# Kernel tuning notes

Hardware: AMD Instinct MI355X
Metric: run time of the kernel (lower is better)

Reference implementation:

```python
import jax, jax.numpy as jnp
import numpy as np

WS = 3   # window_size
ND = 3   # n_degree


def grid_sample_bilinear(x, grid):
    """torch.nn.functional.grid_sample, mode='bilinear', padding_mode='zeros', align_corners=True.
    x: [B,C,H,W]; grid: [B,Hg,Wg,2] with grid[...,0]=x(norm), grid[...,1]=y(norm). -> [B,C,Hg,Wg]"""
    B, C, H, W = x.shape
    gx = (grid[..., 0] + 1.0) * 0.5 * (W - 1)
    gy = (grid[..., 1] + 1.0) * 0.5 * (H - 1)
    x0 = jnp.floor(gx); y0 = jnp.floor(gy)
    x1 = x0 + 1.0;      y1 = y0 + 1.0
    wx1 = gx - x0; wx0 = 1.0 - wx1
    wy1 = gy - y0; wy0 = 1.0 - wy1
    xf = x.reshape(B, C, H * W)

    def gather(yi, xi):
        valid = ((yi >= 0) & (yi <= H - 1) & (xi >= 0) & (xi <= W - 1)).astype(x.dtype)
        yc = jnp.clip(yi, 0, H - 1).astype(jnp.int32)
        xc = jnp.clip(xi, 0, W - 1).astype(jnp.int32)
        idx = yc * W + xc                                   # [B,Hg,Wg]
        v = jax.vmap(lambda xb, ib: jnp.take(xb, ib, axis=1))(xf, idx.reshape(B, -1))
        v = v.reshape(B, C, idx.shape[1], idx.shape[2])      # [B,C,Hg,Wg]
        return v * valid[:, None]

    out = (gather(y0, x0) * (wy0 * wx0)[:, None]
         + gather(y0, x1) * (wy0 * wx1)[:, None]
         + gather(y1, x0) * (wy1 * wx0)[:, None]
         + gather(y1, x1) * (wy1 * wx1)[:, None])
    return out


def setup_inputs() -> dict:
    key = jax.random.key(0)
    ks = jax.random.split(key, 8)
    B, Q, C, H, W = 16, 500, 256, 64, 64
    Np = ND + 1
    query = jax.random.normal(ks[0], (B, Q, C), dtype=jnp.float32)
    # polynomial coefficients kept small so most sample points land inside [-1,1]
    polys = jax.random.uniform(ks[1], (B, Q, 2 * Np), dtype=jnp.float32, minval=0.0, maxval=0.25)
    memory = jax.random.normal(ks[2], (B, H * W, C), dtype=jnp.float32)
    memory_spatial_shapes = np.array([[H, W]], dtype=np.int64)  # static shapes
    Wk = jax.random.normal(ks[3], (C, Np * C, WS, WS), dtype=jnp.float32) * 0.02
    bk = jax.random.normal(ks[4], (C,), dtype=jnp.float32) * 0.02
    Wp = jax.random.normal(ks[5], (C, C), dtype=jnp.float32) * 0.02
    bp = jax.random.normal(ks[6], (C,), dtype=jnp.float32) * 0.02
    return {"query": query, "polys": polys, "memory": memory,
            "memory_spatial_shapes": memory_spatial_shapes,
            "Wk": Wk, "bk": bk, "Wp": Wp, "bp": bp}


def reference(query, polys, memory, memory_spatial_shapes, Wk, bk, Wp, bp):
    B, LEN_V, C = memory.shape
    H = int(memory_spatial_shapes[0][0]); W = int(memory_spatial_shapes[0][1])
    Q = polys.shape[1]
    Np = ND + 1

    # memory -> feature map [B,C,H,W]
    x = jnp.transpose(memory[:, :H * W, :], (0, 2, 1)).reshape(B, C, H, W)

    # polynomial sample points: alphas[s,k] = linspace(0,1)[s] ** (ND-k)
    a = jnp.linspace(0.0, 1.0, Np).astype(polys.dtype)
    A = jnp.stack([a ** i for i in range(ND, -1, -1)], axis=1)          # [Np, Np]
    pts = jnp.einsum('bqck,sk->bqcs', polys.reshape(B, Q, 2, Np), A)    # [B,Q,2,Np]
    pts = jnp.transpose(pts, (0, 1, 3, 2))[..., ::-1]                   # [B,Q,Np,2] (flip coords)
    points = 2.0 * pts - 1.0
    points = points[:, :, None]                                         # [B,Q,1,Np,2]

    # window offsets (note python floor-div: (-3)//2 = -2, matches torch source)
    delta_h = 2.0 * jnp.linspace((-WS) // 2, WS // 2, WS) / H
    delta_w = 2.0 * jnp.linspace((-WS) // 2, WS // 2, WS) / W
    mesh_x, mesh_y = jnp.meshgrid(delta_w, delta_h, indexing='xy')       # [WS,WS]
    mesh_x = mesh_x.reshape(-1, 1); mesh_y = mesh_y.reshape(-1, 1)       # [WS*WS,1]

    grid_x = points[..., 1] + mesh_x                                     # [B,Q,WS*WS,Np]
    grid_y = points[..., 0] + mesh_y
    grid = jnp.stack((grid_y, grid_x), axis=-1)                          # [B,Q,WS*WS,Np,2]
    grid = grid.reshape(B, Q * Np * WS, WS, 2)

    sampled = grid_sample_bilinear(x, grid)                              # [B,C,Q*Np*WS,WS]
    sampled = sampled.reshape(B, C, Q * Np, WS, WS)
    sampled = jnp.transpose(sampled, (0, 2, 1, 3, 4)).reshape(B * Q, Np * C, WS, WS)

    # convkk over full window -> 1x1 output: plain contraction
    crcts = jax.nn.relu(jnp.einsum('nikl,oikl->no', sampled, Wk) + bk)   # [B*Q, C]
    crcts = (crcts @ Wp.T + bp).reshape(B, Q, C)
    return crcts, points
```

## Files before the change

### kernel.cpp

```cpp
#include <hip/hip_runtime.h>

#define NB 16
#define NQ 500
#define NC 256
#define NHW 64
#define MR 8000
#define KD 9216

typedef float f32x4 __attribute__((ext_vector_type(4)));
typedef __bf16 bf16x8 __attribute__((ext_vector_type(8)));
typedef unsigned short ushortx8 __attribute__((ext_vector_type(8)));
typedef unsigned int uintx4 __attribute__((ext_vector_type(4)));
typedef int intx4 __attribute__((ext_vector_type(4)));

__device__ __forceinline__ unsigned short f2bf(float f) {
  unsigned int u = __builtin_bit_cast(unsigned int, f);
  u += 0x7fffu + ((u >> 16) & 1u);
  return (unsigned short)(u >> 16);
}
#define U2F(u) __builtin_bit_cast(float, (unsigned int)(u))

__global__ void k_prep(const float* __restrict__ mem, unsigned short* __restrict__ memb,
                       const float* __restrict__ Wk, const float* __restrict__ Wp,
                       unsigned short* __restrict__ W2s, unsigned short* __restrict__ WPs,
                       const float* __restrict__ polys, float* __restrict__ outp,
                       float* __restrict__ wsp, float* __restrict__ wts) {
  const int bid = blockIdx.x;
  if (bid < 8192) {
    size_t gid = (size_t)bid * 256 + threadIdx.x;
    const float* s = mem + gid * 8;
    f32x4 a = *(const f32x4*)s, b = *(const f32x4*)(s + 4);
    bf16x8 pk;
    pk[0] = (__bf16)a.x; pk[1] = (__bf16)a.y; pk[2] = (__bf16)a.z; pk[3] = (__bf16)a.w;
    pk[4] = (__bf16)b.x; pk[5] = (__bf16)b.y; pk[6] = (__bf16)b.z; pk[7] = (__bf16)b.w;
    *(bf16x8*)(memb + gid * 8) = pk;
  } else if (bid < 9344) {
    int tid = (bid - 8192) * 256 + threadIdx.x;
    int o = tid & 255;
    int th = tid >> 8;
    int r = th >> 5;
    int cbase = (th & 31) * 8;
    int np = r / 9;
    int kl = r - np * 9;
    int kk = kl / 3;
    int ll = kl - kk * 3;
    const float* src = Wk + (size_t)o * KD + (size_t)(np * 256 + cbase) * 9 + kk * 3 + ll;
    ushortx8 v;
#pragma unroll
    for (int j = 0; j < 8; ++j) v[j] = f2bf(src[(size_t)j * 9]);
    *(ushortx8*)(W2s + (size_t)th * 2048 + o * 8) = v;
  } else if (bid < 9376) {
    int tid = (bid - 9344) * 256 + threadIdx.x;
    int o = tid & 255;
    int th = tid >> 8;
    const float* src = Wp + (size_t)o * 256 + th * 8;
    ushortx8 v;
#pragma unroll
    for (int j = 0; j < 8; ++j) v[j] = f2bf(src[j]);
    *(ushortx8*)(WPs + (size_t)th * 2048 + o * 8) = v;
  } else if (bid < 10501) {
    if (!wts) return;
    int e = (bid - 9376) * 256 + threadIdx.x;
    int r = e / 8000;
    int n = e - r * 8000;
    int s = r & 3;
    int mm = r >> 2;
    int mdiv = (mm * 11) >> 5;
    int mmod = mm - 3 * mdiv;
    float dhx = (1.5f * (float)mdiv - 2.0f) * 0.03125f;
    float dwy = (1.5f * (float)mmod - 2.0f) * 0.03125f;
    f32x4 ca = *(const f32x4*)(polys + (size_t)n * 8);
    f32x4 cb = *(const f32x4*)(polys + (size_t)n * 8 + 4);
    float a1 = (s == 3) ? 1.0f : (float)s * 0.33333334f;
    float a2 = a1 * a1, a3 = a2 * a1;
    float v0 = ca.x * a3 + ca.y * a2 + ca.z * a1 + ca.w;
    float v1 = cb.x * a3 + cb.y * a2 + cb.z * a1 + cb.w;
    float p0 = 2.0f * v1 - 1.0f;
    float p1 = 2.0f * v0 - 1.0f;
    const float gx = (p0 + dhx + 1.0f) * 0.5f * 63.0f;
    const float gy = (p1 + dwy + 1.0f) * 0.5f * 63.0f;
    const float x0f = floorf(gx), y0f = floorf(gy);
    const float fx = gx - x0f, fy = gy - y0f;
    const int ix0 = (int)x0f, iy0 = (int)y0f;
    const int ix1 = ix0 + 1, iy1 = iy0 + 1;
    const float vx0 = (ix0 >= 0 && ix0 < NHW) ? 1.0f : 0.0f;
    const float vx1 = (ix1 >= 0 && ix1 < NHW) ? 1.0f : 0.0f;
    const float vy0 = (iy0 >= 0 && iy0 < NHW) ? 1.0f : 0.0f;
    const float vy1 = (iy1 >= 0 && iy1 < NHW) ? 1.0f : 0.0f;
    const float w00 = (1.0f - fy) * (1.0f - fx) * vy0 * vx0;
    const float w01 = (1.0f - fy) * fx * vy0 * vx1;
    const float w10 = fy * (1.0f - fx) * vy1 * vx0;
    const float w11 = fy * fx * vy1 * vx1;
    const int cx0 = min(max(ix0, 0), NHW - 1), cx1 = min(max(ix1, 0), NHW - 1);
    const int cy0 = min(max(iy0, 0), NHW - 1), cy1 = min(max(iy1, 0), NHW - 1);
    float* dst = wts + (size_t)e * 8;
    f32x4 wv; wv.x = w00; wv.y = w01; wv.z = w10; wv.w = w11;
    intx4 ov;
    ov.x = (cy0 * NHW + cx0) * NC; ov.y = (cy0 * NHW + cx1) * NC;
    ov.z = (cy1 * NHW + cx0) * NC; ov.w = (cy1 * NHW + cx1) * NC;
    *(f32x4*)dst = wv;
    *(intx4*)(dst + 4) = ov;
  } else {
    int n = (bid - 10501) * 256 + threadIdx.x;
    if (n >= MR) return;
    f32x4 ca = *(const f32x4*)(polys + (size_t)n * 8);
    f32x4 cb = *(const f32x4*)(polys + (size_t)n * 8 + 4);
    const float av[4] = {0.0f, 0.33333334f, 0.66666669f, 1.0f};
#pragma unroll
    for (int s = 0; s < 4; ++s) {
      float a1 = av[s], a2 = a1 * a1, a3 = a2 * a1;
      float v0 = ca.x * a3 + ca.y * a2 + ca.z * a1 + ca.w;
      float v1 = cb.x * a3 + cb.y * a2 + cb.z * a1 + cb.w;
      float pt0 = 2.0f * v1 - 1.0f;
      float pt1 = 2.0f * v0 - 1.0f;
      outp[(size_t)n * 8 + s * 2 + 0] = pt0;
      outp[(size_t)n * 8 + s * 2 + 1] = pt1;
      wsp[(size_t)n * 8 + s * 2 + 0] = pt0;
      wsp[(size_t)n * 8 + s * 2 + 1] = pt1;
    }
  }
}

template <bool USE_WTS>
__global__ __launch_bounds__(512, 4) void k_gemm1(
    const unsigned short* __restrict__ memb, const float* __restrict__ pts,
    const float* __restrict__ wts, const unsigned short* __restrict__ W2s,
    const float* __restrict__ bk, float* __restrict__ PART, int K) {
  __shared__ __align__(16) unsigned short Alds[2 * 2048 * 8];
  __shared__ __align__(16) float Wlds[2][512];

  const int bid = blockIdx.x;
  const int x = bid & 7;
  const int kk8 = (bid >> 3) % K;
  const int j = bid / (8 * K);
  const int t = x + 8 * j;
  if (t >= 125) return;
  const int tt = 16 * x - ((x > 5) ? (x - 5) : 0) + j;
  const int nsl = 36 / K;
  const int r0 = kk8 * nsl;

  const int tid = threadIdx.x;
  const int n0 = tt * 64;
  const int lane = tid & 63;
  const int wave = tid >> 6;
  const int lr = lane & 15;
  const int ksub = lane >> 4;
  const int o0 = wave * 32;

  const int gchunk = tid & 31;
  const int gm0 = tid >> 5;

  size_t boff[4];
  int nrow[4];
#pragma unroll
  for (int task = 0; task < 4; ++task) {
    nrow[task] = n0 + gm0 + 16 * task;
    boff[task] = (size_t)(nrow[task] / NQ) * (NHW * NHW * NC);
  }

  f32x4 acc[4][2] = {};

  if (USE_WTS) {
    if (tid < 128) {
      f32x4 v = *(const f32x4*)(wts + ((size_t)r0 * 8000 + n0) * 8 + tid * 4);
      *(f32x4*)(&Wlds[0][tid * 4]) = v;
    }
    __syncthreads();
  }

  for (int r = r0; r < r0 + nsl; ++r) {
    const int lbase = ((r - r0) & 1) * 2048;
    const int cur = (r - r0) & 1;
    const int nbuf = cur ^ 1;
    const int rn = (r + 1 < 35) ? (r + 1) : 35;
    float dhx = 0.0f, dwy = 0.0f;
    int s = 0;
    if (!USE_WTS) {
      s = r & 3;
      const int mm = r >> 2;
      const int mdiv = (mm * 11) >> 5;
      const int mmod = mm - 3 * mdiv;
      dhx = (1.5f * (float)mdiv - 2.0f) * 0.03125f;
      dwy = (1.5f * (float)mmod - 2.0f) * 0.03125f;
    } else {
      if (tid < 128) {
        f32x4 v = *(const f32x4*)(wts + ((size_t)rn * 8000 + n0) * 8 + tid * 4);
        *(f32x4*)(&Wlds[nbuf][tid * 4]) = v;
      }
    }
#pragma unroll 2
    for (int task = 0; task < 4; ++task) {
      const int m = gm0 + task * 16;
      const int n = nrow[task];
      float w00, w01, w10, w11;
      int o00, o01, o10, o11;
      if (USE_WTS) {
        const float* we = &Wlds[cur][(gm0 + 16 * task) * 8];
        f32x4 wv = *(const f32x4*)we;
        intx4 ov = *(const intx4*)(we + 4);
        w00 = wv.x; w01 = wv.y; w10 = wv.z; w11 = wv.w;
        o00 = ov.x; o01 = ov.y; o10 = ov.z; o11 = ov.w;
      } else {
        const float p0 = pts[(size_t)n * 8 + s * 2 + 0];
        const float p1 = pts[(size_t)n * 8 + s * 2 + 1];
        const float gx = (p0 + dhx + 1.0f) * 0.5f * 63.0f;
        const float gy = (p1 + dwy + 1.0f) * 0.5f * 63.0f;
        const float x0f = floorf(gx), y0f = floorf(gy);
        const float fx = gx - x0f, fy = gy - y0f;
        const int ix0 = (int)x0f, iy0 = (int)y0f;
        const int ix1 = ix0 + 1, iy1 = iy0 + 1;
        const float vx0 = (ix0 >= 0 && ix0 < NHW) ? 1.0f : 0.0f;
        const float vx1 = (ix1 >= 0 && ix1 < NHW) ? 1.0f : 0.0f;
        const float vy0 = (iy0 >= 0 && iy0 < NHW) ? 1.0f : 0.0f;
        const float vy1 = (iy1 >= 0 && iy1 < NHW) ? 1.0f : 0.0f;
        w00 = (1.0f - fy) * (1.0f - fx) * vy0 * vx0;
        w01 = (1.0f - fy) * fx * vy0 * vx1;
        w10 = fy * (1.0f - fx) * vy1 * vx0;
        w11 = fy * fx * vy1 * vx1;
        const int cx0 = min(max(ix0, 0), NHW - 1), cx1 = min(max(ix1, 0), NHW - 1);
        const int cy0 = min(max(iy0, 0), NHW - 1), cy1 = min(max(iy1, 0), NHW - 1);
        o00 = (cy0 * NHW + cx0) * NC; o01 = (cy0 * NHW + cx1) * NC;
        o10 = (cy1 * NHW + cx0) * NC; o11 = (cy1 * NHW + cx1) * NC;
      }
      const unsigned short* mb = memb + boff[task] + gchunk * 8;
      uintx4 u00 = *(const uintx4*)(mb + o00);
      uintx4 u01 = *(const uintx4*)(mb + o01);
      uintx4 u10 = *(const uintx4*)(mb + o10);
      uintx4 u11 = *(const uintx4*)(mb + o11);
      f32x4 a00, b00, a01, b01, a10, b10, a11, b11;
      a00.x = U2F(u00.x << 16); a00.y = U2F(u00.x & 0xFFFF0000u);
      a00.z = U2F(u00.y << 16); a00.w = U2F(u00.y & 0xFFFF0000u);
      b00.x = U2F(u00.z << 16); b00.y = U2F(u00.z & 0xFFFF0000u);
      b00.z = U2F(u00.w << 16); b00.w = U2F(u00.w & 0xFFFF0000u);
      a01.x = U2F(u01.x << 16); a01.y = U2F(u01.x & 0xFFFF0000u);
      a01.z = U2F(u01.y << 16); a01.w = U2F(u01.y & 0xFFFF0000u);
      b01.x = U2F(u01.z << 16); b01.y = U2F(u01.z & 0xFFFF0000u);
      b01.z = U2F(u01.w << 16); b01.w = U2F(u01.w & 0xFFFF0000u);
      a10.x = U2F(u10.x << 16); a10.y = U2F(u10.x & 0xFFFF0000u);
      a10.z = U2F(u10.y << 16); a10.w = U2F(u10.y & 0xFFFF0000u);
      b10.x = U2F(u10.z << 16); b10.y = U2F(u10.z & 0xFFFF0000u);
      b10.z = U2F(u10.w << 16); b10.w = U2F(u10.w & 0xFFFF0000u);
      a11.x = U2F(u11.x << 16); a11.y = U2F(u11.x & 0xFFFF0000u);
      a11.z = U2F(u11.y << 16); a11.w = U2F(u11.y & 0xFFFF0000u);
      b11.x = U2F(u11.z << 16); b11.y = U2F(u11.z & 0xFFFF0000u);
      b11.z = U2F(u11.w << 16); b11.w = U2F(u11.w & 0xFFFF0000u);
      f32x4 ra = a00 * w00 + a01 * w01 + a10 * w10 + a11 * w11;
      f32x4 rb = b00 * w00 + b01 * w01 + b10 * w10 + b11 * w11;
      bf16x8 pk;
      pk[0] = (__bf16)ra.x; pk[1] = (__bf16)ra.y;
      pk[2] = (__bf16)ra.z; pk[3] = (__bf16)ra.w;
      pk[4] = (__bf16)rb.x; pk[5] = (__bf16)rb.y;
      pk[6] = (__bf16)rb.z; pk[7] = (__bf16)rb.w;
      const int slot = lbase + gchunk * 64 + (m ^ (gchunk & 15));
      *(bf16x8*)(Alds + slot * 8) = pk;
    }
    __syncthreads();
    const size_t rbase = (size_t)r * 32;
#pragma unroll
    for (int kstep = 0; kstep < 8; ++kstep) {
      const int chunk = kstep * 4 + ksub;
      const unsigned short* bp = W2s + (rbase + chunk) * 2048 + (o0 + lr) * 8;
      ushortx8 ub0 = *(const ushortx8*)bp;
      ushortx8 ub1 = *(const ushortx8*)(bp + 128);
      bf16x8 fb0 = __builtin_bit_cast(bf16x8, ub0);
      bf16x8 fb1 = __builtin_bit_cast(bf16x8, ub1);
#pragma unroll
      for (int mf = 0; mf < 4; ++mf) {
        const int sa = lbase + chunk * 64 + ((mf * 16 + lr) ^ (chunk & 15));
        ushortx8 ua = *(const ushortx8*)(Alds + sa * 8);
        bf16x8 fa = __builtin_bit_cast(bf16x8, ua);
        acc[mf][0] = __builtin_amdgcn_mfma_f32_16x16x32_bf16(fa, fb0, acc[mf][0], 0, 0, 0);
        acc[mf][1] = __builtin_amdgcn_mfma_f32_16x16x32_bf16(fa, fb1, acc[mf][1], 0, 0, 0);
      }
    }
  }
  float* dst = PART + (size_t)kk8 * (MR * NC);
#pragma unroll
  for (int mf = 0; mf < 4; ++mf)
#pragma unroll
    for (int nf = 0; nf < 2; ++nf) {
      const int o = o0 + nf * 16 + lr;
#pragma unroll
      for (int reg = 0; reg < 4; ++reg) {
        const int mrow = mf * 16 + ksub * 4 + reg;
        dst[(size_t)(n0 + mrow) * 256 + o] = acc[mf][nf][reg];
      }
    }
}

__global__ __launch_bounds__(256) void k_gemm2(
    const float* __restrict__ PART, const float* __restrict__ bk,
    const unsigned short* __restrict__ WPs, const float* __restrict__ bp,
    float* __restrict__ outc) {
  const int tid = threadIdx.x;
  const int n0 = blockIdx.x * 16;
  const int lane = tid & 63;
  const int wave = tid >> 6;
  const int lr = lane & 15;
  const int ksub = lane >> 4;
  const int o0 = wave * 64;
  f32x4 acc[4] = {};
#pragma unroll
  for (int kstep = 0; kstep < 8; ++kstep) {
    const int t0 = kstep * 32 + ksub * 8;
    const float* base = PART + (size_t)(n0 + lr) * 256 + t0;
    f32x4 s0 = *(const f32x4*)base;
    f32x4 s1 = *(const f32x4*)(base + 4);
#pragma unroll
    for (int k = 1; k < 4; ++k) {
      const float* pk_ = base + (size_t)k * (MR * NC);
      s0 += *(const f32x4*)pk_;
      s1 += *(const f32x4*)(pk_ + 4);
    }
    s0 += *(const f32x4*)(bk + t0);
    s1 += *(const f32x4*)(bk + t0 + 4);
    bf16x8 fa;
#pragma unroll
    for (int e = 0; e < 4; ++e) {
      float v0 = s0[e] > 0.0f ? s0[e] : 0.0f;
      float v1 = s1[e] > 0.0f ? s1[e] : 0.0f;
      fa[e] = (__bf16)v0;
      fa[e + 4] = (__bf16)v1;
    }
    const int chunk = kstep * 4 + ksub;
#pragma unroll
    for (int nf = 0; nf < 4; ++nf) {
      ushortx8 ub = *(const ushortx8*)(WPs + (size_t)chunk * 2048 + (o0 + nf * 16 + lr) * 8);
      bf16x8 fb = __builtin_bit_cast(bf16x8, ub);
      acc[nf] = __builtin_amdgcn_mfma_f32_16x16x32_bf16(fa, fb, acc[nf], 0, 0, 0);
    }
  }
#pragma unroll
  for (int nf = 0; nf < 4; ++nf) {
    const int o = o0 + nf * 16 + lr;
    const float bpo = bp[o];
#pragma unroll
    for (int reg = 0; reg < 4; ++reg) {
      const int mrow = ksub * 4 + reg;
      outc[(size_t)(n0 + mrow) * 256 + o] = acc[nf][reg] + bpo;
    }
  }
}

extern "C" void kernel_launch(void* const* d_in, const int* in_sizes, int n_in,
                              void* d_out, int out_size, void* d_ws, size_t ws_size,
                              hipStream_t stream) {
  (void)in_sizes; (void)n_in; (void)out_size;
  const float* polys = (const float*)d_in[1];
  const float* mem   = (const float*)d_in[2];
  const float* Wk    = (const float*)d_in[4];
  const float* bk    = (const float*)d_in[5];
  const float* Wp    = (const float*)d_in[6];
  const float* bp    = (const float*)d_in[7];
  float* out = (float*)d_out;
  float* out_pts = out + (size_t)MR * NC;

  unsigned short* W2s = (unsigned short*)d_ws;
  unsigned short* WPs = (unsigned short*)((char*)d_ws + 4718592);
  float*          PTS = (float*)((char*)d_ws + 4849664);
  const size_t BASE_END = 9201664;
  const size_t WTS_SZ  = 9216000ull;
  const size_t MEMB_SZ = 33554432ull;
  const size_t PART_SZ = 8192000ull;
  const int K = 4;

  bool use_wts = (ws_size >= BASE_END + WTS_SZ + MEMB_SZ + 4 * PART_SZ);
  size_t memb_off = use_wts ? (BASE_END + WTS_SZ) : BASE_END;
  float*          WTS  = use_wts ? (float*)((char*)d_ws + BASE_END) : nullptr;
  unsigned short* MEMB = (unsigned short*)((char*)d_ws + memb_off);
  float*          PART = (float*)((char*)d_ws + memb_off + MEMB_SZ);

  hipLaunchKernelGGL(k_prep, dim3(10533), dim3(256), 0, stream,
                     mem, MEMB, Wk, Wp, W2s, WPs, polys, out_pts, PTS, WTS);
  if (use_wts)
    hipLaunchKernelGGL(k_gemm1<true>, dim3(128 * K), dim3(512), 0, stream,
                       MEMB, PTS, WTS, W2s, bk, PART, K);
  else
    hipLaunchKernelGGL(k_gemm1<false>, dim3(128 * K), dim3(512), 0, stream,
                       MEMB, PTS, WTS, W2s, bk, PART, K);
  hipLaunchKernelGGL(k_gemm2, dim3(500), dim3(256), 0, stream, PART, bk, WPs, bp, out);
}
```

Before: 104.8 us.

## Use six-way K split with single-buffered LDS when workspace allows

```diff
diff --git a/kernel.cpp b/kernel.cpp
--- a/kernel.cpp
+++ b/kernel.cpp
@@ -121,12 +121,12 @@
   }
 }
 
-template <bool USE_WTS>
+template <bool USE_WTS, int NBUF>
 __global__ __launch_bounds__(512, 4) void k_gemm1(
     const unsigned short* __restrict__ memb, const float* __restrict__ pts,
     const float* __restrict__ wts, const unsigned short* __restrict__ W2s,
     const float* __restrict__ bk, float* __restrict__ PART, int K) {
-  __shared__ __align__(16) unsigned short Alds[2 * 2048 * 8];
+  __shared__ __align__(16) unsigned short Alds[NBUF * 2048 * 8];
   __shared__ __align__(16) float Wlds[2][512];
 
   const int bid = blockIdx.x;
@@ -169,10 +169,11 @@
   }
 
   for (int r = r0; r < r0 + nsl; ++r) {
-    const int lbase = ((r - r0) & 1) * 2048;
+    const int lbase = (NBUF == 2) ? ((r - r0) & 1) * 2048 : 0;
     const int cur = (r - r0) & 1;
     const int nbuf = cur ^ 1;
     const int rn = (r + 1 < 35) ? (r + 1) : 35;
+    if (NBUF == 1 && r != r0) __syncthreads();
     float dhx = 0.0f, dwy = 0.0f;
     int s = 0;
     if (!USE_WTS) {
@@ -291,7 +292,7 @@
 __global__ __launch_bounds__(256) void k_gemm2(
     const float* __restrict__ PART, const float* __restrict__ bk,
     const unsigned short* __restrict__ WPs, const float* __restrict__ bp,
-    float* __restrict__ outc) {
+    float* __restrict__ outc, int K) {
   const int tid = threadIdx.x;
   const int n0 = blockIdx.x * 16;
   const int lane = tid & 63;
@@ -306,8 +307,7 @@
     const float* base = PART + (size_t)(n0 + lr) * 256 + t0;
     f32x4 s0 = *(const f32x4*)base;
     f32x4 s1 = *(const f32x4*)(base + 4);
-#pragma unroll
-    for (int k = 1; k < 4; ++k) {
+    for (int k = 1; k < K; ++k) {
       const float* pk_ = base + (size_t)k * (MR * NC);
       s0 += *(const f32x4*)pk_;
       s1 += *(const f32x4*)(pk_ + 4);
@@ -362,9 +362,10 @@
   const size_t WTS_SZ  = 9216000ull;
   const size_t MEMB_SZ = 33554432ull;
   const size_t PART_SZ = 8192000ull;
-  const int K = 4;
 
   bool use_wts = (ws_size >= BASE_END + WTS_SZ + MEMB_SZ + 4 * PART_SZ);
+  bool k6 = use_wts && (ws_size >= BASE_END + WTS_SZ + MEMB_SZ + 6 * PART_SZ);
+  int K = k6 ? 6 : 4;
   size_t memb_off = use_wts ? (BASE_END + WTS_SZ) : BASE_END;
   float*          WTS  = use_wts ? (float*)((char*)d_ws + BASE_END) : nullptr;
   unsigned short* MEMB = (unsigned short*)((char*)d_ws + memb_off);
@@ -372,11 +373,14 @@
 
   hipLaunchKernelGGL(k_prep, dim3(10533), dim3(256), 0, stream,
                      mem, MEMB, Wk, Wp, W2s, WPs, polys, out_pts, PTS, WTS);
-  if (use_wts)
-    hipLaunchKernelGGL(k_gemm1<true>, dim3(128 * K), dim3(512), 0, stream,
-                       MEMB, PTS, WTS, W2s, bk, PART, K);
+  if (k6)
+    hipLaunchKernelGGL((k_gemm1<true, 1>), dim3(128 * 6), dim3(512), 0, stream,
+                       MEMB, PTS, WTS, W2s, bk, PART, 6);
+  else if (use_wts)
+    hipLaunchKernelGGL((k_gemm1<true, 2>), dim3(128 * 4), dim3(512), 0, stream,
+                       MEMB, PTS, WTS, W2s, bk, PART, 4);
   else
-    hipLaunchKernelGGL(k_gemm1<false>, dim3(128 * K), dim3(512), 0, stream,
-                       MEMB, PTS, WTS, W2s, bk, PART, K);
-  hipLaunchKernelGGL(k_gemm2, dim3(500), dim3(256), 0, stream, PART, bk, WPs, bp, out);
-}
+    hipLaunchKernelGGL((k_gemm1<false, 2>), dim3(128 * 4), dim3(512), 0, stream,
+                       MEMB, PTS, WTS, W2s, bk, PART, 4);
+  hipLaunchKernelGGL(k_gemm2, dim3(500), dim3(256), 0, stream, PART, bk, WPs, bp, out, K);
+}
```

Result: slower. 124.2 us (+18.6%).
